# Optimization experiments

Hardware: AMD Instinct MI355X
Metric: run time of the kernel (lower is better)

Reference implementation:

```python
import jax, jax.numpy as jnp
import numpy as np

NUM_USERS = 500000
NUM_LAYERS = 3
AUDIO_SCALE = 1.0
METADATA_SCALE = 0.5
EPS = 1e-12


def _l2norm(x):
    # matches F.normalize(p=2, dim=-1, eps=1e-12): x / max(||x||, eps)
    n = jnp.sqrt(jnp.sum(x * x, axis=-1, keepdims=True))
    return x / jnp.maximum(n, EPS)


def setup_inputs() -> dict:
    key = jax.random.key(0)
    ks = jax.random.split(key, 12)
    N_SUB, E, D = 131072, 2097152, 64
    NUM_ITEMS, NUM_ARTISTS, NUM_ALBUMS = 500000, 50000, 100000
    batch_nodes = jax.random.randint(ks[0], (N_SUB,), 0, NUM_USERS + NUM_ITEMS, dtype=jnp.int64 if jax.config.jax_enable_x64 else jnp.int32)
    edge_index_sub = jax.random.randint(ks[1], (2, E), 0, N_SUB)
    edge_weight_init_sub = jax.random.uniform(ks[2], (E,), dtype=jnp.float32)
    user_emb_w = jax.random.normal(ks[3], (NUM_USERS, D), dtype=jnp.float32)
    artist_emb_w = jax.random.normal(ks[4], (NUM_ARTISTS, D), dtype=jnp.float32) * 0.05
    album_emb_w = jax.random.normal(ks[5], (NUM_ALBUMS, D), dtype=jnp.float32) * 0.05
    item_audio_emb = jax.random.normal(ks[6], (NUM_ITEMS, D), dtype=jnp.float32)
    artist_ids = jax.random.randint(ks[7], (NUM_ITEMS,), 0, NUM_ARTISTS)
    album_ids = jax.random.randint(ks[8], (NUM_ITEMS,), 0, NUM_ALBUMS)
    proj_w = jax.random.normal(ks[9], (2 * D, D), dtype=jnp.float32) * 0.05
    proj_b = jnp.zeros((D,), dtype=jnp.float32)
    return {
        'batch_nodes': batch_nodes,
        'edge_index_sub': edge_index_sub,
        'edge_weight_init_sub': edge_weight_init_sub,
        'user_emb_w': user_emb_w,
        'artist_emb_w': artist_emb_w,
        'album_emb_w': album_emb_w,
        'item_audio_emb': item_audio_emb,
        'artist_ids': artist_ids,
        'album_ids': album_ids,
        'proj_w': proj_w,
        'proj_b': proj_b,
    }


def reference(batch_nodes, edge_index_sub, edge_weight_init_sub,
              user_emb_w, artist_emb_w, album_emb_w, item_audio_emb,
              artist_ids, album_ids, proj_w, proj_b):
    N = batch_nodes.shape[0]
    row, col = edge_index_sub[0], edge_index_sub[1]

    # add_remaining_self_loops(fill_value=1.0): keep existing edges, append a
    # self-loop for every node; nodes that already have a self-loop get weight 0
    # for the appended loop (a zero-weight edge contributes nothing to deg or
    # aggregation, so this is mathematically identical to PyG's behavior).
    has_loop = jax.ops.segment_sum((row == col).astype(jnp.float32), row, num_segments=N) > 0
    loop_w = jnp.where(has_loop, 0.0, 1.0)
    ar = jnp.arange(N, dtype=row.dtype)
    row_f = jnp.concatenate([row, ar])
    col_f = jnp.concatenate([col, ar])
    w_f = jnp.concatenate([edge_weight_init_sub, loop_w])

    # gcn_norm: deg over targets, symmetric normalization
    deg = jax.ops.segment_sum(w_f, col_f, num_segments=N)
    dinv = jnp.where(deg > 0, jax.lax.rsqrt(jnp.maximum(deg, EPS)), 0.0)
    norm = dinv[row_f] * w_f * dinv[col_f]  # [E+N]

    # node features: users -> normalized user embedding; items -> projected
    user_mask = batch_nodes < NUM_USERS
    u_idx = jnp.where(user_mask, batch_nodes, 0)
    i_idx = jnp.where(user_mask, 0, batch_nodes - NUM_USERS)

    user_e = _l2norm(user_emb_w[u_idx])  # [N, D]
    audio_part = item_audio_emb[i_idx] * AUDIO_SCALE
    meta_part = (artist_emb_w[artist_ids[i_idx]] + album_emb_w[album_ids[i_idx]]) * METADATA_SCALE
    item_e = _l2norm(jnp.concatenate([audio_part, meta_part], axis=-1) @ proj_w + proj_b)

    x = jnp.where(user_mask[:, None], user_e, item_e)  # [N, D]

    # LightGCN propagation: mean over layer-0..num_layers embeddings
    acc = x
    for _ in range(NUM_LAYERS):
        msg = norm[:, None] * x[row_f]              # [E+N, D] gather
        x = jax.ops.segment_sum(msg, col_f, num_segments=N)  # scatter-add
        acc = acc + x
    out = _l2norm(acc / (NUM_LAYERS + 1))
    return out
```

## Files before the change

### kernel.cpp

```cpp
#include <hip/hip_runtime.h>

#define NUM_USERS_C 500000
#define EPS_F 1e-12f

__global__ void k_edgeprep(const int* __restrict__ row, const int* __restrict__ col,
                           int* __restrict__ flags, int* __restrict__ cnt,
                           int* __restrict__ slot, int E) {
    int e = blockIdx.x * blockDim.x + threadIdx.x;
    if (e < E) {
        int r = row[e], c = col[e];
        if (r == c) flags[r] = 1;
        slot[e] = atomicAdd(&cnt[c], 1);
    }
}

__global__ __launch_bounds__(256) void k_blocksum(const int* __restrict__ cnt,
                                                  int* __restrict__ bsum, int N) {
    __shared__ int s[256];
    int i = blockIdx.x * 256 + threadIdx.x;
    s[threadIdx.x] = (i < N) ? cnt[i] : 0;
    __syncthreads();
    for (int d = 128; d > 0; d >>= 1) {
        if (threadIdx.x < d) s[threadIdx.x] += s[threadIdx.x + d];
        __syncthreads();
    }
    if (threadIdx.x == 0) bsum[blockIdx.x] = s[0];
}

__global__ __launch_bounds__(1024) void k_scanbsum(const int* __restrict__ bsum,
                                                   int* __restrict__ boff,
                                                   int* __restrict__ rowptr,
                                                   int NB, int N) {
    __shared__ int s[1024];
    int t = threadIdx.x;
    int v = (t < NB) ? bsum[t] : 0;
    s[t] = v;
    __syncthreads();
    for (int d = 1; d < 1024; d <<= 1) {
        int u = (t >= d) ? s[t - d] : 0;
        __syncthreads();
        s[t] += u;
        __syncthreads();
    }
    if (t < NB) boff[t] = s[t] - v;
    if (t == 1023) rowptr[N] = s[1023];
}

__global__ __launch_bounds__(256) void k_rowptr(const int* __restrict__ cnt,
                                                const int* __restrict__ boff,
                                                int* __restrict__ rowptr, int N) {
    __shared__ int s[256];
    int i = blockIdx.x * 256 + threadIdx.x;
    int v = (i < N) ? cnt[i] : 0;
    s[threadIdx.x] = v;
    __syncthreads();
    for (int d = 1; d < 256; d <<= 1) {
        int u = (threadIdx.x >= d) ? s[threadIdx.x - d] : 0;
        __syncthreads();
        s[threadIdx.x] += u;
        __syncthreads();
    }
    if (i < N) rowptr[i] = boff[blockIdx.x] + s[threadIdx.x] - v;
}

__global__ void k_scatter(const int* __restrict__ row, const int* __restrict__ col,
                          const float* __restrict__ w, const int* __restrict__ slot,
                          const int* __restrict__ rowptr,
                          int2* __restrict__ emeta, int E) {
    int e = blockIdx.x * blockDim.x + threadIdx.x;
    if (e < E) {
        int c = col[e];
        int pos = rowptr[c] + slot[e];
        emeta[pos] = make_int2(row[e], __float_as_int(w[e]));
    }
}

__global__ __launch_bounds__(256) void k_deg(const int* __restrict__ rowptr,
                                             const int2* __restrict__ emeta,
                                             const int* __restrict__ flags,
                                             float2* __restrict__ dinfo, int N) {
    int lane = threadIdx.x & 63;
    int node = blockIdx.x * 4 + (threadIdx.x >> 6);
    if (node >= N) return;
    int beg = rowptr[node], end = rowptr[node + 1];
    float s = 0.0f;
    for (int i = beg + lane; i < end; i += 64)
        s += __int_as_float(emeta[i].y);
    #pragma unroll
    for (int off = 32; off > 0; off >>= 1) s += __shfl_xor(s, off, 64);
    float lw = flags[node] ? 0.0f : 1.0f;
    float d = s + lw;
    float di = (d > 0.0f) ? rsqrtf(fmaxf(d, EPS_F)) : 0.0f;
    if (lane == 0) dinfo[node] = make_float2(di, lw);
}

__device__ __forceinline__ float bcast(float v, int k) {
    return __int_as_float(__builtin_amdgcn_readlane(__float_as_int(v), k));
}

__global__ __launch_bounds__(256) void k_features(
    const int* __restrict__ batch_nodes,
    const float* __restrict__ user_emb, const float* __restrict__ artist_emb,
    const float* __restrict__ album_emb, const float* __restrict__ audio_emb,
    const int* __restrict__ artist_ids, const int* __restrict__ album_ids,
    const float* __restrict__ proj_w, const float* __restrict__ proj_b,
    const float2* __restrict__ dinfo,
    float* __restrict__ xt, float* __restrict__ acc, int N)
{
    __shared__ float Ws[128 * 64];
    for (int i = threadIdx.x; i < 128 * 64; i += blockDim.x)
        Ws[i] = proj_w[i];
    __syncthreads();

    const int lane = threadIdx.x & 63;
    const int wid = threadIdx.x >> 6;
    const int wavesPerBlock = blockDim.x >> 6;
    const int gwid = blockIdx.x * wavesPerBlock + wid;
    const int waveStride = gridDim.x * wavesPerBlock;
    const float bias = proj_b[lane];

    for (int base = gwid * 4; base < N; base += waveStride * 4) {
        float vlo[4], vhi[4], uval[4];
        bool isUser[4];

        #pragma unroll
        for (int j = 0; j < 4; ++j) {
            vlo[j] = 0.0f; vhi[j] = 0.0f; uval[j] = 0.0f; isUser[j] = true;
            if (base + j < N) {
                int idx = batch_nodes[base + j];
                if (idx < NUM_USERS_C) {
                    uval[j] = user_emb[(size_t)idx * 64 + lane];
                } else {
                    isUser[j] = false;
                    int it = idx - NUM_USERS_C;
                    int aid = artist_ids[it];
                    int bid = album_ids[it];
                    vlo[j] = audio_emb[(size_t)it * 64 + lane];
                    vhi[j] = 0.5f * (artist_emb[(size_t)aid * 64 + lane] +
                                     album_emb[(size_t)bid * 64 + lane]);
                }
            }
        }

        float sA[4], sB[4];
        #pragma unroll
        for (int j = 0; j < 4; ++j) { sA[j] = bias; sB[j] = 0.0f; }

        bool anyItem = !(isUser[0] && isUser[1] && isUser[2] && isUser[3]);
        if (anyItem) {
            #pragma unroll
            for (int k = 0; k < 64; k += 2) {
                float w0 = Ws[k * 64 + lane];
                float w1 = Ws[(k + 1) * 64 + lane];
                #pragma unroll
                for (int j = 0; j < 4; ++j) {
                    sA[j] = fmaf(bcast(vlo[j], k),     w0, sA[j]);
                    sB[j] = fmaf(bcast(vlo[j], k + 1), w1, sB[j]);
                }
            }
            #pragma unroll
            for (int k = 0; k < 64; k += 2) {
                float w0 = Ws[(64 + k) * 64 + lane];
                float w1 = Ws[(65 + k) * 64 + lane];
                #pragma unroll
                for (int j = 0; j < 4; ++j) {
                    sA[j] = fmaf(bcast(vhi[j], k),     w0, sA[j]);
                    sB[j] = fmaf(bcast(vhi[j], k + 1), w1, sB[j]);
                }
            }
        }

        #pragma unroll
        for (int j = 0; j < 4; ++j) {
            if (base + j < N) {
                float val = isUser[j] ? uval[j] : (sA[j] + sB[j]);
                float ss = val * val;
                #pragma unroll
                for (int off = 32; off > 0; off >>= 1) ss += __shfl_xor(ss, off, 64);
                float scale = 1.0f / fmaxf(sqrtf(ss), EPS_F);
                val *= scale;
                int n = base + j;
                float di = dinfo[n].x;
                acc[(size_t)n * 64 + lane] = val;
                xt[(size_t)n * 64 + lane] = di * val;
            }
        }
    }
}

__device__ __forceinline__ float prop_accum(
    const int* __restrict__ rowptr, const int2* __restrict__ emeta,
    const float* __restrict__ xs, int node, int lane, float lw)
{
    int beg = rowptr[node], end = rowptr[node + 1];
    float a = lw * xs[(size_t)node * 64 + lane];
    for (int base = beg; base < end; base += 64) {
        int chunk = min(64, end - base);
        int2 m = make_int2(0, 0);
        if (lane < chunk) m = emeta[base + lane];
        int j = 0;
        for (; j + 8 <= chunk; j += 8) {
            int r0 = __shfl(m.x, j + 0); float w0 = __int_as_float(__shfl(m.y, j + 0));
            int r1 = __shfl(m.x, j + 1); float w1 = __int_as_float(__shfl(m.y, j + 1));
            int r2 = __shfl(m.x, j + 2); float w2 = __int_as_float(__shfl(m.y, j + 2));
            int r3 = __shfl(m.x, j + 3); float w3 = __int_as_float(__shfl(m.y, j + 3));
            int r4 = __shfl(m.x, j + 4); float w4 = __int_as_float(__shfl(m.y, j + 4));
            int r5 = __shfl(m.x, j + 5); float w5 = __int_as_float(__shfl(m.y, j + 5));
            int r6 = __shfl(m.x, j + 6); float w6 = __int_as_float(__shfl(m.y, j + 6));
            int r7 = __shfl(m.x, j + 7); float w7 = __int_as_float(__shfl(m.y, j + 7));
            float v0 = xs[(size_t)r0 * 64 + lane];
            float v1 = xs[(size_t)r1 * 64 + lane];
            float v2 = xs[(size_t)r2 * 64 + lane];
            float v3 = xs[(size_t)r3 * 64 + lane];
            float v4 = xs[(size_t)r4 * 64 + lane];
            float v5 = xs[(size_t)r5 * 64 + lane];
            float v6 = xs[(size_t)r6 * 64 + lane];
            float v7 = xs[(size_t)r7 * 64 + lane];
            a = fmaf(w0, v0, a); a = fmaf(w1, v1, a);
            a = fmaf(w2, v2, a); a = fmaf(w3, v3, a);
            a = fmaf(w4, v4, a); a = fmaf(w5, v5, a);
            a = fmaf(w6, v6, a); a = fmaf(w7, v7, a);
        }
        for (; j < chunk; j++) {
            int r = __shfl(m.x, j); float wv = __int_as_float(__shfl(m.y, j));
            a = fmaf(wv, xs[(size_t)r * 64 + lane], a);
        }
    }
    return a;
}

__global__ __launch_bounds__(256) void k_prop(
    const int* __restrict__ rowptr, const int2* __restrict__ emeta,
    const float2* __restrict__ dinfo,
    const float* __restrict__ xs, float* __restrict__ xd,
    float* __restrict__ acc, int N)
{
    int lane = threadIdx.x & 63;
    int node = blockIdx.x * 4 + (threadIdx.x >> 6);
    if (node >= N) return;
    float2 dn = dinfo[node];
    float t = prop_accum(rowptr, emeta, xs, node, lane, dn.y);
    float xnext = dn.x * t;
    acc[(size_t)node * 64 + lane] += xnext;
    xd[(size_t)node * 64 + lane] = dn.x * xnext;
}

__global__ __launch_bounds__(256) void k_prop_final(
    const int* __restrict__ rowptr, const int2* __restrict__ emeta,
    const float2* __restrict__ dinfo,
    const float* __restrict__ xs, float* __restrict__ acc_out, int N)
{
    int lane = threadIdx.x & 63;
    int node = blockIdx.x * 4 + (threadIdx.x >> 6);
    if (node >= N) return;
    float2 dn = dinfo[node];
    float t = prop_accum(rowptr, emeta, xs, node, lane, dn.y);
    float xnext = dn.x * t;
    float v = (acc_out[(size_t)node * 64 + lane] + xnext) * 0.25f;
    float ss = v * v;
    #pragma unroll
    for (int off = 32; off > 0; off >>= 1) ss += __shfl_xor(ss, off, 64);
    float scale = 1.0f / fmaxf(sqrtf(ss), EPS_F);
    acc_out[(size_t)node * 64 + lane] = v * scale;
}

extern "C" void kernel_launch(void* const* d_in, const int* in_sizes, int n_in,
                              void* d_out, int out_size, void* d_ws, size_t ws_size,
                              hipStream_t stream) {
    const int*   batch_nodes = (const int*)d_in[0];
    const int*   edge_index  = (const int*)d_in[1];
    const float* edge_w      = (const float*)d_in[2];
    const float* user_emb    = (const float*)d_in[3];
    const float* artist_emb  = (const float*)d_in[4];
    const float* album_emb   = (const float*)d_in[5];
    const float* audio_emb   = (const float*)d_in[6];
    const int*   artist_ids  = (const int*)d_in[7];
    const int*   album_ids   = (const int*)d_in[8];
    const float* proj_w      = (const float*)d_in[9];
    const float* proj_b      = (const float*)d_in[10];

    const int N = in_sizes[0];
    const int E = in_sizes[2];
    const int* row = edge_index;
    const int* col = edge_index + E;
    float* out = (float*)d_out;

    const int NB = (N + 255) / 256;

    char* ws = (char*)d_ws;
    int*    flags  = (int*)ws;    ws += (size_t)N * sizeof(int);
    int*    cnt    = (int*)ws;    ws += (size_t)N * sizeof(int);
    int*    rowptr = (int*)ws;    ws += (size_t)(N + 1) * sizeof(int);
    int*    bsum   = (int*)ws;    ws += (size_t)NB * sizeof(int);
    int*    boff   = (int*)ws;    ws += (size_t)NB * sizeof(int);
    ws = (char*)(((uintptr_t)ws + 15) & ~(uintptr_t)15);
    float2* dinfo  = (float2*)ws; ws += (size_t)N * sizeof(float2);
    int2*   emeta  = (int2*)ws;   ws += (size_t)E * sizeof(int2);
    float*  xA     = (float*)ws;  ws += (size_t)N * 64 * sizeof(float);
    float*  xB     = (float*)ws;  ws += (size_t)N * 64 * sizeof(float);
    int*    slot   = (int*)xB;

    hipMemsetAsync(flags, 0, (size_t)N * sizeof(int), stream);
    hipMemsetAsync(cnt, 0, (size_t)N * sizeof(int), stream);

    const int TB = 256;

    k_edgeprep<<<(E + TB - 1) / TB, TB, 0, stream>>>(row, col, flags, cnt, slot, E);
    k_blocksum<<<NB, 256, 0, stream>>>(cnt, bsum, N);
    k_scanbsum<<<1, 1024, 0, stream>>>(bsum, boff, rowptr, NB, N);
    k_rowptr<<<NB, 256, 0, stream>>>(cnt, boff, rowptr, N);
    k_scatter<<<(E + TB - 1) / TB, TB, 0, stream>>>(row, col, edge_w, slot,
                                                    rowptr, emeta, E);

    int pblocks = (N + 3) / 4;
    k_deg<<<pblocks, 256, 0, stream>>>(rowptr, emeta, flags, dinfo, N);

    k_features<<<4096, 256, 0, stream>>>(batch_nodes, user_emb, artist_emb, album_emb,
                                         audio_emb, artist_ids, album_ids, proj_w, proj_b,
                                         dinfo, xA, out, N);

    k_prop<<<pblocks, 256, 0, stream>>>(rowptr, emeta, dinfo, xA, xB, out, N);
    k_prop<<<pblocks, 256, 0, stream>>>(rowptr, emeta, dinfo, xB, xA, out, N);
    k_prop_final<<<pblocks, 256, 0, stream>>>(rowptr, emeta, dinfo, xA, out, N);
}
```

Measured before the change: 885.3 us.

## Split feature kernel into user/item paths with per-thread item projection

Nodes are first classified with atomic counters into separate user and item lists. Users are then normalized by a wave-per-node kernel, and items by a kernel that gives each thread one whole item and computes the 128x64 projection in registers, reading weights through uniform loads. The aim is to remove the branch divergence and wasted work of mixing users and items in one wave, and to drop the per-node readlane broadcasts. In exchange it adds two launches, an atomic classify pass, a 64-float accumulator per thread (register pressure) and uncoalesced per-thread row loads.

```diff
diff --git a/kernel.cpp b/kernel.cpp
--- a/kernel.cpp
+++ b/kernel.cpp
@@ -94,96 +94,138 @@
     if (lane == 0) dinfo[node] = make_float2(di, lw);
 }
 
-__device__ __forceinline__ float bcast(float v, int k) {
-    return __int_as_float(__builtin_amdgcn_readlane(__float_as_int(v), k));
-}
-
-__global__ __launch_bounds__(256) void k_features(
-    const int* __restrict__ batch_nodes,
-    const float* __restrict__ user_emb, const float* __restrict__ artist_emb,
-    const float* __restrict__ album_emb, const float* __restrict__ audio_emb,
+__global__ __launch_bounds__(256) void k_classify(const int* __restrict__ batch_nodes,
+                                                  int* __restrict__ ucnt, int* __restrict__ icnt,
+                                                  int* __restrict__ upos, int* __restrict__ ubid,
+                                                  int* __restrict__ ipos, int* __restrict__ iit,
+                                                  int N) {
+    int i = blockIdx.x * 256 + threadIdx.x;
+    if (i >= N) return;
+    int idx = batch_nodes[i];
+    if (idx < NUM_USERS_C) {
+        int p = atomicAdd(ucnt, 1);
+        upos[p] = i; ubid[p] = idx;
+    } else {
+        int p = atomicAdd(icnt, 1);
+        ipos[p] = i; iit[p] = idx - NUM_USERS_C;
+    }
+}
+
+__global__ __launch_bounds__(256) void k_feat_user(
+    const int* __restrict__ ucnt, const int* __restrict__ upos, const int* __restrict__ ubid,
+    const float* __restrict__ user_emb, const float2* __restrict__ dinfo,
+    float* __restrict__ xt, float* __restrict__ acc)
+{
+    int lane = threadIdx.x & 63;
+    int gwid = blockIdx.x * 4 + (threadIdx.x >> 6);
+    int stride = gridDim.x * 4;
+    int uc = *ucnt;
+    for (int u = gwid; u < uc; u += stride) {
+        int n = upos[u];
+        int id = ubid[u];
+        float val = user_emb[(size_t)id * 64 + lane];
+        float ss = val * val;
+        #pragma unroll
+        for (int off = 32; off > 0; off >>= 1) ss += __shfl_xor(ss, off, 64);
+        float scale = 1.0f / fmaxf(sqrtf(ss), EPS_F);
+        val *= scale;
+        float di = dinfo[n].x;
+        acc[(size_t)n * 64 + lane] = val;
+        xt[(size_t)n * 64 + lane] = di * val;
+    }
+}
+
+__device__ __forceinline__ void fma8(float* __restrict__ a64,
+                                     const float* __restrict__ proj_w,
+                                     float4 x0, float4 x1, int kb) {
+    const float xs[8] = {x0.x, x0.y, x0.z, x0.w, x1.x, x1.y, x1.z, x1.w};
+    #pragma unroll
+    for (int jj = 0; jj < 8; jj++) {
+        const float* wr = proj_w + (size_t)(kb + jj) * 64;
+        float av = xs[jj];
+        #pragma unroll
+        for (int d = 0; d < 64; d++) a64[d] = fmaf(av, wr[d], a64[d]);
+    }
+}
+
+__device__ __forceinline__ float4 avg2(float4 a, float4 b) {
+    float4 r;
+    r.x = 0.5f * (a.x + b.x); r.y = 0.5f * (a.y + b.y);
+    r.z = 0.5f * (a.z + b.z); r.w = 0.5f * (a.w + b.w);
+    return r;
+}
+
+__global__ __launch_bounds__(256) void k_feat_item(
+    const int* __restrict__ icnt, const int* __restrict__ ipos, const int* __restrict__ iit,
+    const float* __restrict__ artist_emb, const float* __restrict__ album_emb,
+    const float* __restrict__ audio_emb,
     const int* __restrict__ artist_ids, const int* __restrict__ album_ids,
     const float* __restrict__ proj_w, const float* __restrict__ proj_b,
     const float2* __restrict__ dinfo,
-    float* __restrict__ xt, float* __restrict__ acc, int N)
-{
-    __shared__ float Ws[128 * 64];
-    for (int i = threadIdx.x; i < 128 * 64; i += blockDim.x)
-        Ws[i] = proj_w[i];
-    __syncthreads();
-
+    float* __restrict__ xt, float* __restrict__ acc)
+{
     const int lane = threadIdx.x & 63;
-    const int wid = threadIdx.x >> 6;
-    const int wavesPerBlock = blockDim.x >> 6;
-    const int gwid = blockIdx.x * wavesPerBlock + wid;
-    const int waveStride = gridDim.x * wavesPerBlock;
-    const float bias = proj_b[lane];
-
-    for (int base = gwid * 4; base < N; base += waveStride * 4) {
-        float vlo[4], vhi[4], uval[4];
-        bool isUser[4];
-
+    const int gwid = blockIdx.x * 4 + (threadIdx.x >> 6);
+    const int ic = *icnt;
+    const int base = gwid * 64;
+    if (base >= ic) return;
+    int j = base + lane;
+    bool live = j < ic;
+    int jj = live ? j : (ic - 1);
+    int n  = ipos[jj];
+    int it = iit[jj];
+    int aid = artist_ids[it];
+    int bid = album_ids[it];
+    const float4* __restrict__ A = (const float4*)(audio_emb  + (size_t)it  * 64);
+    const float4* __restrict__ R = (const float4*)(artist_emb + (size_t)aid * 64);
+    const float4* __restrict__ S = (const float4*)(album_emb  + (size_t)bid * 64);
+
+    float a[64];
+    #pragma unroll
+    for (int d = 0; d < 64; d++) a[d] = proj_b[d];
+
+    float4 c0 = A[0], c1 = A[1];
+    #pragma unroll 1
+    for (int kb = 0; kb < 7; kb++) {
+        float4 p0 = A[(kb + 1) * 2], p1 = A[(kb + 1) * 2 + 1];
+        fma8(a, proj_w, c0, c1, kb * 8);
+        c0 = p0; c1 = p1;
+    }
+    float4 r0 = R[0], r1 = R[1], s0 = S[0], s1 = S[1];
+    fma8(a, proj_w, c0, c1, 56);
+
+    #pragma unroll 1
+    for (int kb = 0; kb < 7; kb++) {
+        float4 nr0 = R[(kb + 1) * 2], nr1 = R[(kb + 1) * 2 + 1];
+        float4 ns0 = S[(kb + 1) * 2], ns1 = S[(kb + 1) * 2 + 1];
+        fma8(a, proj_w, avg2(r0, s0), avg2(r1, s1), 64 + kb * 8);
+        r0 = nr0; r1 = nr1; s0 = ns0; s1 = ns1;
+    }
+    fma8(a, proj_w, avg2(r0, s0), avg2(r1, s1), 120);
+
+    float ss0 = 0.0f, ss1 = 0.0f, ss2 = 0.0f, ss3 = 0.0f;
+    #pragma unroll
+    for (int d = 0; d < 64; d += 4) {
+        ss0 = fmaf(a[d + 0], a[d + 0], ss0);
+        ss1 = fmaf(a[d + 1], a[d + 1], ss1);
+        ss2 = fmaf(a[d + 2], a[d + 2], ss2);
+        ss3 = fmaf(a[d + 3], a[d + 3], ss3);
+    }
+    float ss = (ss0 + ss1) + (ss2 + ss3);
+    float scale = 1.0f / fmaxf(sqrtf(ss), EPS_F);
+    float di = dinfo[n].x;
+    if (live) {
+        float4* ao = (float4*)(acc + (size_t)n * 64);
+        float4* xo = (float4*)(xt + (size_t)n * 64);
         #pragma unroll
-        for (int j = 0; j < 4; ++j) {
-            vlo[j] = 0.0f; vhi[j] = 0.0f; uval[j] = 0.0f; isUser[j] = true;
-            if (base + j < N) {
-                int idx = batch_nodes[base + j];
-                if (idx < NUM_USERS_C) {
-                    uval[j] = user_emb[(size_t)idx * 64 + lane];
-                } else {
-                    isUser[j] = false;
-                    int it = idx - NUM_USERS_C;
-                    int aid = artist_ids[it];
-                    int bid = album_ids[it];
-                    vlo[j] = audio_emb[(size_t)it * 64 + lane];
-                    vhi[j] = 0.5f * (artist_emb[(size_t)aid * 64 + lane] +
-                                     album_emb[(size_t)bid * 64 + lane]);
-                }
-            }
-        }
-
-        float sA[4], sB[4];
-        #pragma unroll
-        for (int j = 0; j < 4; ++j) { sA[j] = bias; sB[j] = 0.0f; }
-
-        bool anyItem = !(isUser[0] && isUser[1] && isUser[2] && isUser[3]);
-        if (anyItem) {
-            #pragma unroll
-            for (int k = 0; k < 64; k += 2) {
-                float w0 = Ws[k * 64 + lane];
-                float w1 = Ws[(k + 1) * 64 + lane];
-                #pragma unroll
-                for (int j = 0; j < 4; ++j) {
-                    sA[j] = fmaf(bcast(vlo[j], k),     w0, sA[j]);
-                    sB[j] = fmaf(bcast(vlo[j], k + 1), w1, sB[j]);
-                }
-            }
-            #pragma unroll
-            for (int k = 0; k < 64; k += 2) {
-                float w0 = Ws[(64 + k) * 64 + lane];
-                float w1 = Ws[(65 + k) * 64 + lane];
-                #pragma unroll
-                for (int j = 0; j < 4; ++j) {
-                    sA[j] = fmaf(bcast(vhi[j], k),     w0, sA[j]);
-                    sB[j] = fmaf(bcast(vhi[j], k + 1), w1, sB[j]);
-                }
-            }
-        }
-
-        #pragma unroll
-        for (int j = 0; j < 4; ++j) {
-            if (base + j < N) {
-                float val = isUser[j] ? uval[j] : (sA[j] + sB[j]);
-                float ss = val * val;
-                #pragma unroll
-                for (int off = 32; off > 0; off >>= 1) ss += __shfl_xor(ss, off, 64);
-                float scale = 1.0f / fmaxf(sqrtf(ss), EPS_F);
-                val *= scale;
-                int n = base + j;
-                float di = dinfo[n].x;
-                acc[(size_t)n * 64 + lane] = val;
-                xt[(size_t)n * 64 + lane] = di * val;
-            }
+        for (int d4 = 0; d4 < 16; d4++) {
+            float4 v;
+            v.x = a[d4 * 4 + 0] * scale; v.y = a[d4 * 4 + 1] * scale;
+            v.z = a[d4 * 4 + 2] * scale; v.w = a[d4 * 4 + 3] * scale;
+            ao[d4] = v;
+            float4 w;
+            w.x = v.x * di; w.y = v.y * di; w.z = v.z * di; w.w = v.w * di;
+            xo[d4] = w;
         }
     }
 }
@@ -293,12 +335,18 @@
     int*    rowptr = (int*)ws;    ws += (size_t)(N + 1) * sizeof(int);
     int*    bsum   = (int*)ws;    ws += (size_t)NB * sizeof(int);
     int*    boff   = (int*)ws;    ws += (size_t)NB * sizeof(int);
+    int*    cnts2  = (int*)ws;    ws += 2 * sizeof(int);
     ws = (char*)(((uintptr_t)ws + 15) & ~(uintptr_t)15);
     float2* dinfo  = (float2*)ws; ws += (size_t)N * sizeof(float2);
     int2*   emeta  = (int2*)ws;   ws += (size_t)E * sizeof(int2);
     float*  xA     = (float*)ws;  ws += (size_t)N * 64 * sizeof(float);
     float*  xB     = (float*)ws;  ws += (size_t)N * 64 * sizeof(float);
-    int*    slot   = (int*)xB;
+
+    int* slot = (int*)xB;
+    int* upos = (int*)xB;
+    int* ubid = upos + N;
+    int* ipos = ubid + N;
+    int* iit  = ipos + N;
 
     hipMemsetAsync(flags, 0, (size_t)N * sizeof(int), stream);
     hipMemsetAsync(cnt, 0, (size_t)N * sizeof(int), stream);
@@ -315,9 +363,18 @@
     int pblocks = (N + 3) / 4;
     k_deg<<<pblocks, 256, 0, stream>>>(rowptr, emeta, flags, dinfo, N);
 
-    k_features<<<4096, 256, 0, stream>>>(batch_nodes, user_emb, artist_emb, album_emb,
-                                         audio_emb, artist_ids, album_ids, proj_w, proj_b,
-                                         dinfo, xA, out, N);
+    hipMemsetAsync(cnts2, 0, 2 * sizeof(int), stream);
+    k_classify<<<NB, 256, 0, stream>>>(batch_nodes, &cnts2[0], &cnts2[1],
+                                       upos, ubid, ipos, iit, N);
+
+    k_feat_user<<<1024, 256, 0, stream>>>(&cnts2[0], upos, ubid, user_emb, dinfo, xA, out);
+
+    int iwaves = (N + 63) / 64;
+    int iblocks = (iwaves + 3) / 4;
+    k_feat_item<<<iblocks, 256, 0, stream>>>(&cnts2[1], ipos, iit,
+                                             artist_emb, album_emb, audio_emb,
+                                             artist_ids, album_ids, proj_w, proj_b,
+                                             dinfo, xA, out);
 
     k_prop<<<pblocks, 256, 0, stream>>>(rowptr, emeta, dinfo, xA, xB, out, N);
     k_prop<<<pblocks, 256, 0, stream>>>(rowptr, emeta, dinfo, xB, xA, out, N);
```

Result: slower. 936.8 us (+5.8%).

## Split user/item feature paths and carry scaled states through propagation

Applied to the files above, without the earlier changes.

Batch nodes are first classified into user and item lists with atomics. Users then get a cheap normalize-only kernel, and items run the projection matmul in groups of 8 with no user branches mixed in. The propagation now stores dinv-scaled intermediate states, so acc is computed algebraically instead of via a separate acc initialisation write and per-layer read-modify-write. The gather loop is also unrolled to 16 loads in flight. In exchange it adds extra launches, an atomic compaction pass, and intermediate buffers aliased over xB, and it changes the floating-point order of the accumulation.

```diff
diff --git a/kernel.cpp b/kernel.cpp
--- a/kernel.cpp
+++ b/kernel.cpp
@@ -94,18 +94,56 @@
     if (lane == 0) dinfo[node] = make_float2(di, lw);
 }
 
+__global__ __launch_bounds__(256) void k_classify(const int* __restrict__ batch_nodes,
+                                                  int* __restrict__ ucnt, int* __restrict__ icnt,
+                                                  int* __restrict__ upos, int* __restrict__ ubid,
+                                                  int* __restrict__ ipos, int* __restrict__ iit,
+                                                  int N) {
+    int i = blockIdx.x * 256 + threadIdx.x;
+    if (i >= N) return;
+    int idx = batch_nodes[i];
+    if (idx < NUM_USERS_C) {
+        int p = atomicAdd(ucnt, 1);
+        upos[p] = i; ubid[p] = idx;
+    } else {
+        int p = atomicAdd(icnt, 1);
+        ipos[p] = i; iit[p] = idx - NUM_USERS_C;
+    }
+}
+
+__global__ __launch_bounds__(256) void k_feat_user(
+    const int* __restrict__ ucnt, const int* __restrict__ upos, const int* __restrict__ ubid,
+    const float* __restrict__ user_emb, const float2* __restrict__ dinfo,
+    float* __restrict__ xt)
+{
+    int lane = threadIdx.x & 63;
+    int gwid = blockIdx.x * 4 + (threadIdx.x >> 6);
+    int stride = gridDim.x * 4;
+    int uc = *ucnt;
+    for (int u = gwid; u < uc; u += stride) {
+        int n = upos[u];
+        int id = ubid[u];
+        float val = user_emb[(size_t)id * 64 + lane];
+        float ss = val * val;
+        #pragma unroll
+        for (int off = 32; off > 0; off >>= 1) ss += __shfl_xor(ss, off, 64);
+        float scale = 1.0f / fmaxf(sqrtf(ss), EPS_F);
+        xt[(size_t)n * 64 + lane] = dinfo[n].x * val * scale;
+    }
+}
+
 __device__ __forceinline__ float bcast(float v, int k) {
     return __int_as_float(__builtin_amdgcn_readlane(__float_as_int(v), k));
 }
 
-__global__ __launch_bounds__(256) void k_features(
-    const int* __restrict__ batch_nodes,
-    const float* __restrict__ user_emb, const float* __restrict__ artist_emb,
-    const float* __restrict__ album_emb, const float* __restrict__ audio_emb,
+__global__ __launch_bounds__(256) void k_feat_item(
+    const int* __restrict__ icnt, const int* __restrict__ ipos, const int* __restrict__ iit,
+    const float* __restrict__ artist_emb, const float* __restrict__ album_emb,
+    const float* __restrict__ audio_emb,
     const int* __restrict__ artist_ids, const int* __restrict__ album_ids,
     const float* __restrict__ proj_w, const float* __restrict__ proj_b,
     const float2* __restrict__ dinfo,
-    float* __restrict__ xt, float* __restrict__ acc, int N)
+    float* __restrict__ xt)
 {
     __shared__ float Ws[128 * 64];
     for (int i = threadIdx.x; i < 128 * 64; i += blockDim.x)
@@ -114,112 +152,102 @@
 
     const int lane = threadIdx.x & 63;
     const int wid = threadIdx.x >> 6;
-    const int wavesPerBlock = blockDim.x >> 6;
-    const int gwid = blockIdx.x * wavesPerBlock + wid;
-    const int waveStride = gridDim.x * wavesPerBlock;
+    const int ic = *icnt;
+    const int ngroups = (ic + 7) / 8;
+    const int gstride = gridDim.x * 4;
     const float bias = proj_b[lane];
 
-    for (int base = gwid * 4; base < N; base += waveStride * 4) {
-        float vlo[4], vhi[4], uval[4];
-        bool isUser[4];
-
-        #pragma unroll
-        for (int j = 0; j < 4; ++j) {
-            vlo[j] = 0.0f; vhi[j] = 0.0f; uval[j] = 0.0f; isUser[j] = true;
-            if (base + j < N) {
-                int idx = batch_nodes[base + j];
-                if (idx < NUM_USERS_C) {
-                    uval[j] = user_emb[(size_t)idx * 64 + lane];
-                } else {
-                    isUser[j] = false;
-                    int it = idx - NUM_USERS_C;
-                    int aid = artist_ids[it];
-                    int bid = album_ids[it];
-                    vlo[j] = audio_emb[(size_t)it * 64 + lane];
-                    vhi[j] = 0.5f * (artist_emb[(size_t)aid * 64 + lane] +
-                                     album_emb[(size_t)bid * 64 + lane]);
-                }
-            }
-        }
-
-        float sA[4], sB[4];
-        #pragma unroll
-        for (int j = 0; j < 4; ++j) { sA[j] = bias; sB[j] = 0.0f; }
-
-        bool anyItem = !(isUser[0] && isUser[1] && isUser[2] && isUser[3]);
-        if (anyItem) {
-            #pragma unroll
-            for (int k = 0; k < 64; k += 2) {
-                float w0 = Ws[k * 64 + lane];
-                float w1 = Ws[(k + 1) * 64 + lane];
-                #pragma unroll
-                for (int j = 0; j < 4; ++j) {
-                    sA[j] = fmaf(bcast(vlo[j], k),     w0, sA[j]);
-                    sB[j] = fmaf(bcast(vlo[j], k + 1), w1, sB[j]);
-                }
-            }
-            #pragma unroll
-            for (int k = 0; k < 64; k += 2) {
-                float w0 = Ws[(64 + k) * 64 + lane];
-                float w1 = Ws[(65 + k) * 64 + lane];
-                #pragma unroll
-                for (int j = 0; j < 4; ++j) {
-                    sA[j] = fmaf(bcast(vhi[j], k),     w0, sA[j]);
-                    sB[j] = fmaf(bcast(vhi[j], k + 1), w1, sB[j]);
-                }
-            }
-        }
-
-        #pragma unroll
-        for (int j = 0; j < 4; ++j) {
-            if (base + j < N) {
-                float val = isUser[j] ? uval[j] : (sA[j] + sB[j]);
+    for (int g = blockIdx.x * 4 + wid; g < ngroups; g += gstride) {
+        int base = g * 8;
+        int cnt8 = min(8, ic - base);
+        float vlo[8], vhi[8];
+        int nn[8];
+        #pragma unroll
+        for (int j = 0; j < 8; ++j) {
+            int jj = (j < cnt8) ? base + j : base;
+            int it = iit[jj];
+            nn[j] = ipos[jj];
+            int aid = artist_ids[it];
+            int bid = album_ids[it];
+            vlo[j] = audio_emb[(size_t)it * 64 + lane];
+            vhi[j] = 0.5f * (artist_emb[(size_t)aid * 64 + lane] +
+                             album_emb[(size_t)bid * 64 + lane]);
+        }
+
+        float sA[8], sB[8];
+        #pragma unroll
+        for (int j = 0; j < 8; ++j) { sA[j] = bias; sB[j] = 0.0f; }
+
+        #pragma unroll
+        for (int k = 0; k < 64; k += 2) {
+            float w0 = Ws[k * 64 + lane];
+            float w1 = Ws[(k + 1) * 64 + lane];
+            #pragma unroll
+            for (int j = 0; j < 8; ++j) {
+                sA[j] = fmaf(bcast(vlo[j], k),     w0, sA[j]);
+                sB[j] = fmaf(bcast(vlo[j], k + 1), w1, sB[j]);
+            }
+        }
+        #pragma unroll
+        for (int k = 0; k < 64; k += 2) {
+            float w0 = Ws[(64 + k) * 64 + lane];
+            float w1 = Ws[(65 + k) * 64 + lane];
+            #pragma unroll
+            for (int j = 0; j < 8; ++j) {
+                sA[j] = fmaf(bcast(vhi[j], k),     w0, sA[j]);
+                sB[j] = fmaf(bcast(vhi[j], k + 1), w1, sB[j]);
+            }
+        }
+
+        #pragma unroll
+        for (int j = 0; j < 8; ++j) {
+            if (j < cnt8) {
+                float val = sA[j] + sB[j];
                 float ss = val * val;
                 #pragma unroll
                 for (int off = 32; off > 0; off >>= 1) ss += __shfl_xor(ss, off, 64);
                 float scale = 1.0f / fmaxf(sqrtf(ss), EPS_F);
-                val *= scale;
-                int n = base + j;
-                float di = dinfo[n].x;
-                acc[(size_t)n * 64 + lane] = val;
-                xt[(size_t)n * 64 + lane] = di * val;
-            }
-        }
-    }
-}
-
-__device__ __forceinline__ float prop_accum(
+                int n = nn[j];
+                xt[(size_t)n * 64 + lane] = dinfo[n].x * val * scale;
+            }
+        }
+    }
+}
+
+__device__ __forceinline__ float prop_edges(
     const int* __restrict__ rowptr, const int2* __restrict__ emeta,
-    const float* __restrict__ xs, int node, int lane, float lw)
+    const float* __restrict__ xs, int node, int lane)
 {
     int beg = rowptr[node], end = rowptr[node + 1];
-    float a = lw * xs[(size_t)node * 64 + lane];
+    float a = 0.0f;
     for (int base = beg; base < end; base += 64) {
         int chunk = min(64, end - base);
         int2 m = make_int2(0, 0);
         if (lane < chunk) m = emeta[base + lane];
         int j = 0;
+        for (; j + 16 <= chunk; j += 16) {
+            int rr[16]; float ww[16], vv[16];
+            #pragma unroll
+            for (int t = 0; t < 16; t++) {
+                rr[t] = __shfl(m.x, j + t);
+                ww[t] = __int_as_float(__shfl(m.y, j + t));
+            }
+            #pragma unroll
+            for (int t = 0; t < 16; t++) vv[t] = xs[(size_t)rr[t] * 64 + lane];
+            #pragma unroll
+            for (int t = 0; t < 16; t++) a = fmaf(ww[t], vv[t], a);
+        }
         for (; j + 8 <= chunk; j += 8) {
-            int r0 = __shfl(m.x, j + 0); float w0 = __int_as_float(__shfl(m.y, j + 0));
-            int r1 = __shfl(m.x, j + 1); float w1 = __int_as_float(__shfl(m.y, j + 1));
-            int r2 = __shfl(m.x, j + 2); float w2 = __int_as_float(__shfl(m.y, j + 2));
-            int r3 = __shfl(m.x, j + 3); float w3 = __int_as_float(__shfl(m.y, j + 3));
-            int r4 = __shfl(m.x, j + 4); float w4 = __int_as_float(__shfl(m.y, j + 4));
-            int r5 = __shfl(m.x, j + 5); float w5 = __int_as_float(__shfl(m.y, j + 5));
-            int r6 = __shfl(m.x, j + 6); float w6 = __int_as_float(__shfl(m.y, j + 6));
-            int r7 = __shfl(m.x, j + 7); float w7 = __int_as_float(__shfl(m.y, j + 7));
-            float v0 = xs[(size_t)r0 * 64 + lane];
-            float v1 = xs[(size_t)r1 * 64 + lane];
-            float v2 = xs[(size_t)r2 * 64 + lane];
-            float v3 = xs[(size_t)r3 * 64 + lane];
-            float v4 = xs[(size_t)r4 * 64 + lane];
-            float v5 = xs[(size_t)r5 * 64 + lane];
-            float v6 = xs[(size_t)r6 * 64 + lane];
-            float v7 = xs[(size_t)r7 * 64 + lane];
-            a = fmaf(w0, v0, a); a = fmaf(w1, v1, a);
-            a = fmaf(w2, v2, a); a = fmaf(w3, v3, a);
-            a = fmaf(w4, v4, a); a = fmaf(w5, v5, a);
-            a = fmaf(w6, v6, a); a = fmaf(w7, v7, a);
+            int rr[8]; float ww[8], vv[8];
+            #pragma unroll
+            for (int t = 0; t < 8; t++) {
+                rr[t] = __shfl(m.x, j + t);
+                ww[t] = __int_as_float(__shfl(m.y, j + t));
+            }
+            #pragma unroll
+            for (int t = 0; t < 8; t++) vv[t] = xs[(size_t)rr[t] * 64 + lane];
+            #pragma unroll
+            for (int t = 0; t < 8; t++) a = fmaf(ww[t], vv[t], a);
         }
         for (; j < chunk; j++) {
             int r = __shfl(m.x, j); float wv = __int_as_float(__shfl(m.y, j));
@@ -229,39 +257,58 @@
     return a;
 }
 
-__global__ __launch_bounds__(256) void k_prop(
+__global__ __launch_bounds__(256) void k_prop1(
+    const int* __restrict__ rowptr, const int2* __restrict__ emeta,
+    const float2* __restrict__ dinfo,
+    const float* __restrict__ xs, float* __restrict__ xd, int N)
+{
+    int lane = threadIdx.x & 63;
+    int node = blockIdx.x * 4 + (threadIdx.x >> 6);
+    if (node >= N) return;
+    float2 dn = dinfo[node];
+    float self = xs[(size_t)node * 64 + lane];
+    float t = dn.y * self + prop_edges(rowptr, emeta, xs, node, lane);
+    xd[(size_t)node * 64 + lane] = (dn.x * dn.x) * t;
+}
+
+__global__ __launch_bounds__(256) void k_prop2(
     const int* __restrict__ rowptr, const int2* __restrict__ emeta,
     const float2* __restrict__ dinfo,
     const float* __restrict__ xs, float* __restrict__ xd,
-    float* __restrict__ acc, int N)
+    float* __restrict__ ps, int N)
 {
     int lane = threadIdx.x & 63;
     int node = blockIdx.x * 4 + (threadIdx.x >> 6);
     if (node >= N) return;
     float2 dn = dinfo[node];
-    float t = prop_accum(rowptr, emeta, xs, node, lane, dn.y);
-    float xnext = dn.x * t;
-    acc[(size_t)node * 64 + lane] += xnext;
-    xd[(size_t)node * 64 + lane] = dn.x * xnext;
+    size_t o = (size_t)node * 64 + lane;
+    float s1 = xs[o];
+    float t = dn.y * s1 + prop_edges(rowptr, emeta, xs, node, lane);
+    float x2t = (dn.x * dn.x) * t;
+    xd[o] = x2t;
+    ps[o] = ps[o] + s1 + x2t;
 }
 
 __global__ __launch_bounds__(256) void k_prop_final(
     const int* __restrict__ rowptr, const int2* __restrict__ emeta,
     const float2* __restrict__ dinfo,
-    const float* __restrict__ xs, float* __restrict__ acc_out, int N)
+    const float* __restrict__ xs, const float* __restrict__ ps,
+    float* __restrict__ out, int N)
 {
     int lane = threadIdx.x & 63;
     int node = blockIdx.x * 4 + (threadIdx.x >> 6);
     if (node >= N) return;
     float2 dn = dinfo[node];
-    float t = prop_accum(rowptr, emeta, xs, node, lane, dn.y);
-    float xnext = dn.x * t;
-    float v = (acc_out[(size_t)node * 64 + lane] + xnext) * 0.25f;
+    size_t o = (size_t)node * 64 + lane;
+    float s2 = xs[o];
+    float t = dn.y * s2 + prop_edges(rowptr, emeta, xs, node, lane);
+    float x3t = (dn.x * dn.x) * t;
+    float v = ps[o] + x3t;
     float ss = v * v;
     #pragma unroll
     for (int off = 32; off > 0; off >>= 1) ss += __shfl_xor(ss, off, 64);
     float scale = 1.0f / fmaxf(sqrtf(ss), EPS_F);
-    acc_out[(size_t)node * 64 + lane] = v * scale;
+    out[o] = v * scale;
 }
 
 extern "C" void kernel_launch(void* const* d_in, const int* in_sizes, int n_in,
@@ -293,12 +340,18 @@
     int*    rowptr = (int*)ws;    ws += (size_t)(N + 1) * sizeof(int);
     int*    bsum   = (int*)ws;    ws += (size_t)NB * sizeof(int);
     int*    boff   = (int*)ws;    ws += (size_t)NB * sizeof(int);
+    int*    cnts2  = (int*)ws;    ws += 2 * sizeof(int);
     ws = (char*)(((uintptr_t)ws + 15) & ~(uintptr_t)15);
     float2* dinfo  = (float2*)ws; ws += (size_t)N * sizeof(float2);
     int2*   emeta  = (int2*)ws;   ws += (size_t)E * sizeof(int2);
     float*  xA     = (float*)ws;  ws += (size_t)N * 64 * sizeof(float);
     float*  xB     = (float*)ws;  ws += (size_t)N * 64 * sizeof(float);
-    int*    slot   = (int*)xB;
+
+    int* slot = (int*)xB;
+    int* upos = (int*)xB;
+    int* ubid = upos + N;
+    int* ipos = ubid + N;
+    int* iit  = ipos + N;
 
     hipMemsetAsync(flags, 0, (size_t)N * sizeof(int), stream);
     hipMemsetAsync(cnt, 0, (size_t)N * sizeof(int), stream);
@@ -315,11 +368,17 @@
     int pblocks = (N + 3) / 4;
     k_deg<<<pblocks, 256, 0, stream>>>(rowptr, emeta, flags, dinfo, N);
 
-    k_features<<<4096, 256, 0, stream>>>(batch_nodes, user_emb, artist_emb, album_emb,
-                                         audio_emb, artist_ids, album_ids, proj_w, proj_b,
-                                         dinfo, xA, out, N);
-
-    k_prop<<<pblocks, 256, 0, stream>>>(rowptr, emeta, dinfo, xA, xB, out, N);
-    k_prop<<<pblocks, 256, 0, stream>>>(rowptr, emeta, dinfo, xB, xA, out, N);
-    k_prop_final<<<pblocks, 256, 0, stream>>>(rowptr, emeta, dinfo, xA, out, N);
-}
+    hipMemsetAsync(cnts2, 0, 2 * sizeof(int), stream);
+    k_classify<<<NB, 256, 0, stream>>>(batch_nodes, &cnts2[0], &cnts2[1],
+                                       upos, ubid, ipos, iit, N);
+
+    k_feat_user<<<1024, 256, 0, stream>>>(&cnts2[0], upos, ubid, user_emb, dinfo, xA);
+    k_feat_item<<<4096, 256, 0, stream>>>(&cnts2[1], ipos, iit,
+                                          artist_emb, album_emb, audio_emb,
+                                          artist_ids, album_ids, proj_w, proj_b,
+                                          dinfo, xA);
+
+    k_prop1<<<pblocks, 256, 0, stream>>>(rowptr, emeta, dinfo, xA, out, N);
+    k_prop2<<<pblocks, 256, 0, stream>>>(rowptr, emeta, dinfo, out, xB, xA, N);
+    k_prop_final<<<pblocks, 256, 0, stream>>>(rowptr, emeta, dinfo, xB, xA, out, N);
+}
```

New measurement: 925.9 us. 4.6% more time.
